# Optimization experiments

Measured on AMD Instinct MI355X. Metric: run time of the kernel, lower is better.

Reference implementation:

```python
import jax, jax.numpy as jnp
import numpy as np
from jax import lax

B, T, C, H = 4, 2048, 512, 8
HD = C // H
FF = 4 * C

def _ln(x, g, b, eps=1e-5):
    m = jnp.mean(x, -1, keepdims=True)
    v = jnp.var(x, -1, keepdims=True)
    return (x - m) * lax.rsqrt(v + eps) * g + b

def setup_inputs():
    key = jax.random.key(0)
    ks = jax.random.split(key, 16)
    n = lambda i, shape, s=0.02: jax.random.normal(ks[i], shape, jnp.float32) * s
    return dict(
        x=jax.random.normal(ks[0], (B, T, C), jnp.float32),
        A=jax.random.uniform(ks[1], (B, T), dtype=jnp.float32),
        alpha_bias=jnp.full((1,), 0.1, jnp.float32),
        dst_alpha=jnp.asarray(0.7, jnp.float32),
        dst_beta=jnp.asarray(0.3, jnp.float32),
        conv1_w=n(2, (C, C, 3)), conv1_b=jnp.zeros((C,), jnp.float32),
        ln1_g=jnp.ones((C,), jnp.float32), ln1_b=jnp.zeros((C,), jnp.float32),
        in_proj_w=n(3, (3 * C, C)), in_proj_b=jnp.zeros((3 * C,), jnp.float32),
        out_w=n(4, (C, C)), out_b=jnp.zeros((C,), jnp.float32),
        ln2_g=jnp.ones((C,), jnp.float32), ln2_b=jnp.zeros((C,), jnp.float32),
        mlp_w1=n(5, (FF, C)), mlp_b1=jnp.zeros((FF,), jnp.float32),
        mlp_w2=n(6, (C, FF)), mlp_b2=jnp.zeros((C,), jnp.float32),
        dsa_ln_g=jnp.ones((C,), jnp.float32), dsa_ln_b=jnp.zeros((C,), jnp.float32),
        dsa_dw=n(7, (C, 1, 3)), dsa_db=jnp.zeros((C,), jnp.float32),
        dsa_pw=n(8, (C, C, 1)), dsa_pb=jnp.zeros((C,), jnp.float32),
    )

def reference(x, A, alpha_bias, dst_alpha, dst_beta, conv1_w, conv1_b, ln1_g, ln1_b,
              in_proj_w, in_proj_b, out_w, out_b, ln2_g, ln2_b,
              mlp_w1, mlp_b1, mlp_w2, mlp_b2,
              dsa_ln_g, dsa_ln_b, dsa_dw, dsa_db, dsa_pw, dsa_pb):
    dn = ('NCH', 'OIH', 'NCH')
    # --- CA branch: conv pre-mix on [B,C,T] with residual ---
    xT = jnp.transpose(x, (0, 2, 1))                       # [B,C,T]
    y = lax.conv_general_dilated(xT, conv1_w, (1,), [(1, 1)], dimension_numbers=dn) + conv1_b[None, :, None]
    Ftc = jnp.transpose(xT + jax.nn.gelu(y, approximate=False), (0, 2, 1))  # [B,T,C]
    h = _ln(Ftc, ln1_g, ln1_b)
    # --- MHA with rank-1 additive boundary bias alpha * A_i A_j (detached) ---
    qkv = h @ in_proj_w.T + in_proj_b
    q, k, v = jnp.split(qkv, 3, axis=-1)
    q = q.reshape(B, T, H, HD)
    k = k.reshape(B, T, H, HD)
    v = v.reshape(B, T, H, HD)
    scores = jnp.einsum('bihd,bjhd->bhij', q, k) / np.float32(np.sqrt(HD))
    M_bias = lax.stop_gradient(A[:, :, None] * A[:, None, :])  # [B,T,T]
    scores = scores + (alpha_bias[0] * M_bias)[:, None]        # broadcast over heads
    p = jax.nn.softmax(scores, axis=-1)
    attn = jnp.einsum('bhij,bjhd->bihd', p, v).reshape(B, T, C)
    attn = attn @ out_w.T + out_b
    Ftc2 = attn + x
    hh = _ln(Ftc2, ln2_g, ln2_b)
    ca_out = jax.nn.gelu(hh @ mlp_w1.T + mlp_b1, approximate=False) @ mlp_w2.T + mlp_b2
    # --- DSA branch: depthwise-separable temporal conv ---
    z = _ln(x, dsa_ln_g, dsa_ln_b)
    zT = jnp.transpose(z, (0, 2, 1))
    z1 = lax.conv_general_dilated(zT, dsa_dw, (1,), [(1, 1)], dimension_numbers=dn, feature_group_count=C) + dsa_db[None, :, None]
    z2 = lax.conv_general_dilated(jax.nn.gelu(z1, approximate=False), dsa_pw, (1,), [(0, 0)], dimension_numbers=dn) + dsa_pb[None, :, None]
    dsa_out = jnp.transpose(z2, (0, 2, 1))
    return dst_alpha * ca_out + dst_beta * dsa_out
```

## Files before the change

kernel.cpp:

```cpp
#include <hip/hip_runtime.h>
#include <cmath>

typedef __attribute__((ext_vector_type(8))) short short8;
typedef __attribute__((ext_vector_type(4))) float floatx4;

#define TT 2048
#define CCH 512
#define MROWS 8192
static const size_t N1 = 4194304;
#define LOG2E 1.44269504088896340736f

__device__ __forceinline__ float gelu_f(float x) {
    return 0.5f * x * (1.0f + erff(x * 0.70710678118654752440f));
}
__device__ __forceinline__ unsigned short f2bf(float x) {
    union { float f; unsigned u; } v; v.f = x;
    unsigned r = v.u + 0x7fffu + ((v.u >> 16) & 1u);
    return (unsigned short)(r >> 16);
}
__device__ __forceinline__ float bf2f(unsigned short h) {
    union { unsigned u; float f; } v; v.u = ((unsigned)h) << 16;
    return v.f;
}
__device__ __forceinline__ unsigned cvtpk(float a, float b) {
    unsigned r;
    asm("v_cvt_pk_bf16_f32 %0, %1, %2" : "=v"(r) : "v"(a), "v"(b));
    return r;
}
__device__ __forceinline__ void gld16(const unsigned short* g, unsigned short* l) {
    __builtin_amdgcn_global_load_lds(
        (const __attribute__((address_space(1))) void*)g,
        (__attribute__((address_space(3))) void*)l, 16, 0, 0);
}

__global__ __launch_bounds__(256)
void pack_w(const float* __restrict__ qkvw, const float* __restrict__ outw,
            const float* __restrict__ w1, const float* __restrict__ w2,
            const float* __restrict__ pw, const float* __restrict__ cv,
            unsigned short* __restrict__ W)
{
    const int idx = blockIdx.x * 256 + threadIdx.x;
    float v;
    if (idx < 786432)            v = qkvw[idx];
    else if (idx < 1048576)      v = outw[idx - 786432];
    else if (idx < 2097152)      v = w1[idx - 1048576];
    else if (idx < 3145728)      v = w2[idx - 2097152];
    else if (idx < 3407872)      v = pw[idx - 3145728];
    else {
        const int l = idx - 3407872;
        const int n = l / 1536, k = l - n * 1536;
        const int ks = k >> 9, ci = k & 511;
        v = cv[n * 1536 + ci * 3 + ks];
    }
    W[idx] = f2bf(v);
}

__global__ __launch_bounds__(256)
void pack_x(const float* __restrict__ x, const float* __restrict__ gam,
            const float* __restrict__ bet, unsigned short* __restrict__ z,
            unsigned short* __restrict__ xpad)
{
    const int m = blockIdx.x, tid = threadIdx.x;
    const int b = m >> 11, t = m & (TT - 1);
    const float2 xv = *(const float2*)&x[(size_t)m * 512 + 2 * tid];
    float s = xv.x + xv.y, sq = xv.x * xv.x + xv.y * xv.y;
    #pragma unroll
    for (int off = 32; off; off >>= 1) { s += __shfl_xor(s, off); sq += __shfl_xor(sq, off); }
    __shared__ float ws[4], wq[4];
    const int wave = tid >> 6, lane = tid & 63;
    if (lane == 0) { ws[wave] = s; wq[wave] = sq; }
    __syncthreads();
    s = ws[0] + ws[1] + ws[2] + ws[3];
    sq = wq[0] + wq[1] + wq[2] + wq[3];
    const float mean = s * (1.0f / 512.0f);
    const float var = sq * (1.0f / 512.0f) - mean * mean;
    const float rstd = rsqrtf(var + 1e-5f);
    const float y0 = (xv.x - mean) * rstd * gam[2 * tid]     + bet[2 * tid];
    const float y1 = (xv.y - mean) * rstd * gam[2 * tid + 1] + bet[2 * tid + 1];
    *(unsigned*)&z[(size_t)m * 512 + 2 * tid] = ((unsigned)f2bf(y1) << 16) | f2bf(y0);
    *(unsigned*)&xpad[((size_t)(b * (TT + 2) + t + 1)) * 512 + 2 * tid] =
        ((unsigned)f2bf(xv.y) << 16) | f2bf(xv.x);
    if (t == 0)
        *(unsigned*)&xpad[((size_t)(b * (TT + 2))) * 512 + 2 * tid] = 0u;
    if (t == TT - 1)
        *(unsigned*)&xpad[((size_t)(b * (TT + 2) + TT + 1)) * 512 + 2 * tid] = 0u;
}

__global__ __launch_bounds__(256)
void ln_bf(const unsigned short* __restrict__ in, const float* __restrict__ gam,
           const float* __restrict__ bet, unsigned short* __restrict__ out)
{
    const int m = blockIdx.x, tid = threadIdx.x;
    const unsigned pv = *(const unsigned*)&in[(size_t)m * 512 + 2 * tid];
    const float x0 = bf2f((unsigned short)pv), x1 = bf2f((unsigned short)(pv >> 16));
    float s = x0 + x1, sq = x0 * x0 + x1 * x1;
    #pragma unroll
    for (int off = 32; off; off >>= 1) { s += __shfl_xor(s, off); sq += __shfl_xor(sq, off); }
    __shared__ float ws[4], wq[4];
    const int wave = tid >> 6, lane = tid & 63;
    if (lane == 0) { ws[wave] = s; wq[wave] = sq; }
    __syncthreads();
    s = ws[0] + ws[1] + ws[2] + ws[3];
    sq = wq[0] + wq[1] + wq[2] + wq[3];
    const float mean = s * (1.0f / 512.0f);
    const float var = sq * (1.0f / 512.0f) - mean * mean;
    const float rstd = rsqrtf(var + 1e-5f);
    const float y0 = (x0 - mean) * rstd * gam[2 * tid]     + bet[2 * tid];
    const float y1 = (x1 - mean) * rstd * gam[2 * tid + 1] + bet[2 * tid + 1];
    *(unsigned*)&out[(size_t)m * 512 + 2 * tid] = ((unsigned)f2bf(y1) << 16) | f2bf(y0);
}

__global__ __launch_bounds__(256)
void dwconv_k(const unsigned short* __restrict__ z, const float* __restrict__ dw,
              const float* __restrict__ db, unsigned short* __restrict__ g)
{
    const int m = blockIdx.x, tid = threadIdx.x, t = m & (TT - 1);
    const int c = 2 * tid;
    const size_t base = (size_t)m * 512 + c;
    const unsigned vm = *(const unsigned*)&z[base];
    const unsigned va = (t > 0)      ? *(const unsigned*)&z[base - 512] : 0u;
    const unsigned vc = (t < TT - 1) ? *(const unsigned*)&z[base + 512] : 0u;
    float y[2];
    #pragma unroll
    for (int j = 0; j < 2; ++j) {
        const float a  = bf2f((unsigned short)(va >> (16 * j)));
        const float bb = bf2f((unsigned short)(vm >> (16 * j)));
        const float cc = bf2f((unsigned short)(vc >> (16 * j)));
        const int ch = c + j;
        y[j] = gelu_f(a * dw[ch * 3] + bb * dw[ch * 3 + 1] + cc * dw[ch * 3 + 2] + db[ch]);
    }
    *(unsigned*)&g[base] = ((unsigned)f2bf(y[1]) << 16) | f2bf(y[0]);
}

template<int EPI, int AF>
__device__ __forceinline__ void gemm_body(
    const unsigned short* __restrict__ A, const unsigned short* __restrict__ Bw,
    const float* __restrict__ bias, const float* __restrict__ resf,
    const unsigned short* __restrict__ dsa,
    const float* __restrict__ sA, const float* __restrict__ sB,
    float* __restrict__ outf, unsigned short* __restrict__ o1,
    unsigned short* __restrict__ o2, unsigned short* __restrict__ o3,
    int Nn, int K, int gx, unsigned short* AsB, unsigned short* BsB)
{
    constexpr int MI = 4, NJ = 2, NBUF = 2;
    constexpr int ASTR = 64 * 32, BSTR = 128 * 32;

    const int nwg = gx * gridDim.y;
    const int orig = blockIdx.x + gx * blockIdx.y;
    const int wg = (orig & 7) * (nwg >> 3) + (orig >> 3);
    const int bx = wg % gx, by = wg / gx;

    const int tid = threadIdx.x;
    const int bm = by * 64, bn = bx * 128;
    const int lane = tid & 63, w = tid >> 6;
    const int wc = w;
    const int lr = lane & 15, g = lane >> 4;

    auto stage = [&](int buf, int k0) {
        unsigned short* Asb = AsB + buf * ASTR;
        unsigned short* Bsb = BsB + buf * BSTR;
        {
            const int c = tid;
            const int r = c >> 2, c8 = c & 3;
            const int c8s = c8 ^ ((r >> 1) & 3);
            const unsigned short* src;
            if (AF == 1) {
                const int m = bm + r;
                const int b = m >> 11, t = m & (TT - 1);
                const int k = k0 + c8s * 8;
                const int ks = k >> 9, ci = k & 511;
                src = A + ((size_t)(b * (TT + 2) + t + ks) * 512 + ci);
            } else {
                src = A + ((size_t)(bm + r) * K + k0 + c8s * 8);
            }
            gld16(src, Asb + (size_t)c * 8);
        }
        #pragma unroll
        for (int i = 0; i < 2; ++i) {
            const int c = tid + i * 256;
            const int r = c >> 2, c8 = c & 3;
            const int c8s = c8 ^ ((r >> 1) & 3);
            gld16(Bw + ((size_t)(bn + r) * K + k0 + c8s * 8), Bsb + (size_t)c * 8);
        }
    };

    floatx4 acc[MI][NJ];
    #pragma unroll
    for (int mi = 0; mi < MI; ++mi)
        #pragma unroll
        for (int nj = 0; nj < NJ; ++nj)
            acc[mi][nj] = (floatx4){0.f, 0.f, 0.f, 0.f};

    const int nt = K >> 5;
    stage(0, 0);
    __syncthreads();
    int cur = 0;
    for (int t = 0; t < nt; ++t) {
        if (t + 1 < nt) stage(cur ^ 1, (t + 1) * 32);

        const unsigned short* Asb = AsB + cur * ASTR;
        const unsigned short* Bsb = BsB + cur * BSTR;
        short8 av[MI], bv[NJ];
        #pragma unroll
        for (int mi = 0; mi < MI; ++mi) {
            const int row = mi * 16 + lr;
            av[mi] = *(const short8*)&Asb[row * 32 + (g ^ ((row >> 1) & 3)) * 8];
        }
        #pragma unroll
        for (int nj = 0; nj < NJ; ++nj) {
            const int row = wc * 32 + nj * 16 + lr;
            bv[nj] = *(const short8*)&Bsb[row * 32 + (g ^ ((row >> 1) & 3)) * 8];
        }
        __builtin_amdgcn_s_setprio(1);
        #pragma unroll
        for (int mi = 0; mi < MI; ++mi)
            #pragma unroll
            for (int nj = 0; nj < NJ; ++nj)
                acc[mi][nj] = __builtin_amdgcn_mfma_f32_16x16x32_bf16(av[mi], bv[nj], acc[mi][nj], 0, 0, 0);
        __builtin_amdgcn_s_setprio(0);
        __syncthreads();
        cur ^= 1;
    }

    float sa = 0.f, sb = 0.f;
    if (EPI == 5) { sa = sA[0]; sb = sB[0]; }
    #pragma unroll
    for (int mi = 0; mi < MI; ++mi)
        #pragma unroll
        for (int nj = 0; nj < NJ; ++nj)
            #pragma unroll
            for (int reg = 0; reg < 4; ++reg) {
                const int m = bm + mi * 16 + g * 4 + reg;
                const int n = bn + wc * 32 + nj * 16 + lr;
                float v = acc[mi][nj][reg] + bias[n];
                if (EPI == 0) {
                    const int b = m >> 11, t = m & (TT - 1);
                    if (n < 512) {
                        o1[(size_t)m * 512 + n] = f2bf(v * (0.125f * LOG2E));
                    } else if (n < 1024) {
                        o2[(size_t)m * 512 + (n - 512)] = f2bf(v);
                    } else {
                        const int c = n - 1024;
                        o3[(size_t)(b * 8 + (c >> 6)) * 64 * TT + (size_t)(c & 63) * TT + t] = f2bf(v);
                    }
                } else if (EPI == 1) {
                    o1[(size_t)m * 512 + n] = f2bf(v);
                } else if (EPI == 2) {
                    o1[(size_t)m * 512 + n] = f2bf(resf[(size_t)m * 512 + n] + gelu_f(v));
                } else if (EPI == 3) {
                    o1[(size_t)m * 512 + n] = f2bf(v + resf[(size_t)m * 512 + n]);
                } else if (EPI == 4) {
                    o1[(size_t)m * Nn + n] = f2bf(gelu_f(v));
                } else {
                    outf[(size_t)m * 512 + n] = sa * v + sb * bf2f(dsa[(size_t)m * 512 + n]);
                }
            }
}

template<int EPI, int AF>
__global__ __launch_bounds__(256, 4)
void gemm_k(const unsigned short* __restrict__ A, const unsigned short* __restrict__ Bw,
            const float* __restrict__ bias, const float* __restrict__ resf,
            const unsigned short* __restrict__ dsa,
            const float* __restrict__ sA, const float* __restrict__ sB,
            float* __restrict__ outf, unsigned short* __restrict__ o1,
            unsigned short* __restrict__ o2, unsigned short* __restrict__ o3,
            int Nn, int K)
{
    __shared__ unsigned short As[2 * 64 * 32];
    __shared__ unsigned short Bs[2 * 128 * 32];
    gemm_body<EPI, AF>(A, Bw, bias, resf, dsa, sA, sB, outf, o1, o2, o3,
                       Nn, K, gridDim.x, As, Bs);
}

__global__ __launch_bounds__(256, 4)
void gemm_dual(const unsigned short* __restrict__ Gb, const unsigned short* __restrict__ Wpw,
               const float* __restrict__ dsa_pb, unsigned short* __restrict__ Db,
               const unsigned short* __restrict__ xpad, const unsigned short* __restrict__ Wcv,
               const float* __restrict__ conv1_b, const float* __restrict__ x,
               unsigned short* __restrict__ U1)
{
    __shared__ unsigned short As[2 * 64 * 32];
    __shared__ unsigned short Bs[2 * 128 * 32];
    if (blockIdx.z == 0)
        gemm_body<1, 0>(Gb, Wpw, dsa_pb, nullptr, nullptr, nullptr, nullptr,
                        nullptr, Db, nullptr, nullptr, 512, 512, gridDim.x, As, Bs);
    else
        gemm_body<2, 1>(xpad, Wcv, conv1_b, x, nullptr, nullptr, nullptr,
                        nullptr, U1, nullptr, nullptr, 512, 1536, gridDim.x, As, Bs);
}

__global__ __launch_bounds__(512, 2)
void attn_k(const unsigned short* __restrict__ Qb, const unsigned short* __restrict__ Kb,
            const unsigned short* __restrict__ Vtg, const float* __restrict__ Avec,
            const float* __restrict__ alpha_p, unsigned short* __restrict__ Oh)
{
    __shared__ unsigned short Kt[2][2][64 * 64];
    __shared__ unsigned short Vt[2][2][64 * 64];
    __shared__ unsigned short P2[8][16 * 64];

    const int tid = threadIdx.x;
    const int w = tid >> 6, lane = tid & 63;
    const int lr = lane & 15, g = lane >> 4;
    const int i0 = blockIdx.x * 128;
    const int h = blockIdx.y, b = blockIdx.z;
    const float* Ab = Avec + b * TT;
    const int q_glob = i0 + w * 16 + lr;
    const float aqs = alpha_p[0] * LOG2E * Ab[q_glob];

    const int j_s = tid >> 3, c8_s = tid & 7;

    short8 kreg[2], vreg[2];
    auto load_tiles = [&](int kv0) {
        #pragma unroll
        for (int i = 0; i < 2; ++i) {
            kreg[i] = *(const short8*)&Kb[(size_t)(b * TT + kv0 + i * 64 + j_s) * 512 + h * 64 + c8_s * 8];
            vreg[i] = *(const short8*)&Vtg[(size_t)((b * 8 + h) * 64 + j_s) * TT + kv0 + i * 64 + c8_s * 8];
        }
    };
    auto write_tiles = [&](int buf) {
        const int off = j_s * 64 + (((c8_s * 16) ^ ((j_s & 7) << 4)) >> 1);
        #pragma unroll
        for (int i = 0; i < 2; ++i) {
            *(short8*)&Kt[buf][i][off] = kreg[i];
            *(short8*)&Vt[buf][i][off] = vreg[i];
        }
    };

    short8 qf[2];
    #pragma unroll
    for (int kk = 0; kk < 2; ++kk)
        qf[kk] = *(const short8*)&Qb[(size_t)(b * TT + q_glob) * 512 + h * 64 + kk * 32 + g * 8];

    float l_part = 0.f;
    floatx4 o[4];
    #pragma unroll
    for (int fd = 0; fd < 4; ++fd) o[fd] = (floatx4){0.f, 0.f, 0.f, 0.f};

    load_tiles(0);
    write_tiles(0);
    __syncthreads();
    int cur = 0;

    for (int t = 0; t < 16; ++t) {
        if (t < 15) load_tiles((t + 1) * 128);

        #pragma unroll
        for (int st = 0; st < 2; ++st) {
            const int kv0 = t * 128 + st * 64;

            floatx4 akv[4];
            #pragma unroll
            for (int fc = 0; fc < 4; ++fc)
                akv[fc] = *(const floatx4*)&Ab[kv0 + fc * 16 + g * 4];

            floatx4 s[4];
            #pragma unroll
            for (int fc = 0; fc < 4; ++fc) {
                const int row = fc * 16 + lr;
                const short8 kf0 = *(const short8*)&Kt[cur][st][row * 64 + (((g * 16) ^ ((row & 7) << 4)) >> 1)];
                const short8 kf1 = *(const short8*)&Kt[cur][st][row * 64 + (((64 + g * 16) ^ ((row & 7) << 4)) >> 1)];
                floatx4 tacc = (floatx4){0.f, 0.f, 0.f, 0.f};
                __builtin_amdgcn_s_setprio(1);
                tacc = __builtin_amdgcn_mfma_f32_16x16x32_bf16(kf0, qf[0], tacc, 0, 0, 0);
                tacc = __builtin_amdgcn_mfma_f32_16x16x32_bf16(kf1, qf[1], tacc, 0, 0, 0);
                __builtin_amdgcn_s_setprio(0);
                s[fc] = tacc;
            }
            #pragma unroll
            for (int fc = 0; fc < 4; ++fc)
                #pragma unroll
                for (int r = 0; r < 4; ++r) {
                    const float p = exp2f(s[fc][r] + aqs * akv[fc][r]);
                    s[fc][r] = p;
                    l_part += p;
                }

            #pragma unroll
            for (int fc = 0; fc < 4; ++fc) {
                uint2 pk;
                pk.x = cvtpk(s[fc][0], s[fc][1]);
                pk.y = cvtpk(s[fc][2], s[fc][3]);
                const int boff = (lr * 128 + fc * 32 + g * 8) ^ ((lr & 7) << 4);
                *(uint2*)((char*)&P2[w][0] + boff) = pk;
            }
            short8 pf[2];
            #pragma unroll
            for (int kk = 0; kk < 2; ++kk) {
                const int boff = (lr * 128 + kk * 64 + g * 16) ^ ((lr & 7) << 4);
                pf[kk] = *(const short8*)((const char*)&P2[w][0] + boff);
            }
            #pragma unroll
            for (int fd = 0; fd < 4; ++fd) {
                const int row = fd * 16 + lr;
                const short8 vf0 = *(const short8*)&Vt[cur][st][row * 64 + (((g * 16) ^ ((row & 7) << 4)) >> 1)];
                const short8 vf1 = *(const short8*)&Vt[cur][st][row * 64 + (((64 + g * 16) ^ ((row & 7) << 4)) >> 1)];
                __builtin_amdgcn_s_setprio(1);
                o[fd] = __builtin_amdgcn_mfma_f32_16x16x32_bf16(vf0, pf[0], o[fd], 0, 0, 0);
                o[fd] = __builtin_amdgcn_mfma_f32_16x16x32_bf16(vf1, pf[1], o[fd], 0, 0, 0);
                __builtin_amdgcn_s_setprio(0);
            }
        }

        if (t < 15) write_tiles(cur ^ 1);
        __syncthreads();
        cur ^= 1;
    }

    l_part += __shfl_xor(l_part, 16);
    l_part += __shfl_xor(l_part, 32);
    const float inv = 1.0f / l_part;
    const size_t orow = (size_t)(b * TT + q_glob) * 512 + h * 64;
    #pragma unroll
    for (int fd = 0; fd < 4; ++fd) {
        uint2 pk;
        pk.x = cvtpk(o[fd][0] * inv, o[fd][1] * inv);
        pk.y = cvtpk(o[fd][2] * inv, o[fd][3] * inv);
        *(uint2*)&Oh[orow + fd * 16 + g * 4] = pk;
    }
}

extern "C" void kernel_launch(void* const* d_in, const int* in_sizes, int n_in,
                              void* d_out, int out_size, void* d_ws, size_t ws_size,
                              hipStream_t stream)
{
    const float* x         = (const float*)d_in[0];
    const float* Avec      = (const float*)d_in[1];
    const float* alpha_b   = (const float*)d_in[2];
    const float* dst_alpha = (const float*)d_in[3];
    const float* dst_beta  = (const float*)d_in[4];
    const float* conv1_w   = (const float*)d_in[5];
    const float* conv1_b   = (const float*)d_in[6];
    const float* ln1_g     = (const float*)d_in[7];
    const float* ln1_b     = (const float*)d_in[8];
    const float* in_proj_w = (const float*)d_in[9];
    const float* in_proj_b = (const float*)d_in[10];
    const float* out_w     = (const float*)d_in[11];
    const float* out_b     = (const float*)d_in[12];
    const float* ln2_g     = (const float*)d_in[13];
    const float* ln2_b     = (const float*)d_in[14];
    const float* mlp_w1    = (const float*)d_in[15];
    const float* mlp_b1    = (const float*)d_in[16];
    const float* mlp_w2    = (const float*)d_in[17];
    const float* mlp_b2    = (const float*)d_in[18];
    const float* dsa_ln_g  = (const float*)d_in[19];
    const float* dsa_ln_b  = (const float*)d_in[20];
    const float* dsa_dw    = (const float*)d_in[21];
    const float* dsa_db    = (const float*)d_in[22];
    const float* dsa_pw    = (const float*)d_in[23];
    const float* dsa_pb    = (const float*)d_in[24];

    unsigned short* W    = (unsigned short*)d_ws;
    unsigned short* xpad = W + N1;
    unsigned short* Qb   = xpad + (size_t)4 * (TT + 2) * 512;
    unsigned short* Kbf  = Qb + N1;
    unsigned short* Vt   = Kbf + N1;
    unsigned short* Zb   = Vt + N1;
    unsigned short* Tb   = Qb;
    unsigned short* Gb   = Zb + N1;
    unsigned short* Db   = Gb + N1;
    unsigned short* U1   = Db + N1;
    unsigned short* U2   = U1 + N1;
    unsigned short* U3   = U2 + N1;

    const int off_qkv = 0, off_out = 786432, off_w1 = 1048576,
              off_w2 = 2097152, off_pw = 3145728, off_cv = 3407872;

    pack_w<<<16384, 256, 0, stream>>>(in_proj_w, out_w, mlp_w1, mlp_w2, dsa_pw, conv1_w, W);
    pack_x<<<MROWS, 256, 0, stream>>>(x, dsa_ln_g, dsa_ln_b, Zb, xpad);

    dwconv_k<<<MROWS, 256, 0, stream>>>(Zb, dsa_dw, dsa_db, Gb);
    gemm_dual<<<dim3(4, 128, 2), 256, 0, stream>>>(Gb, W + off_pw, dsa_pb, Db,
        xpad, W + off_cv, conv1_b, x, U1);
    ln_bf<<<MROWS, 256, 0, stream>>>(U1, ln1_g, ln1_b, U2);

    gemm_k<0, 0><<<dim3(12, 128), 256, 0, stream>>>(U2, W + off_qkv, in_proj_b,
        nullptr, nullptr, nullptr, nullptr, nullptr, Qb, Kbf, Vt, 1536, 512);

    attn_k<<<dim3(16, 8, 4), 512, 0, stream>>>(Qb, Kbf, Vt, Avec, alpha_b, U1);

    gemm_k<3, 0><<<dim3(4, 128), 256, 0, stream>>>(U1, W + off_out, out_b,
        x, nullptr, nullptr, nullptr, nullptr, U3, nullptr, nullptr, 512, 512);
    ln_bf<<<MROWS, 256, 0, stream>>>(U3, ln2_g, ln2_b, U2);

    gemm_k<4, 0><<<dim3(16, 128), 256, 0, stream>>>(U2, W + off_w1, mlp_b1,
        nullptr, nullptr, nullptr, nullptr, nullptr, Tb, nullptr, nullptr, 2048, 512);
    gemm_k<5, 0><<<dim3(4, 128), 256, 0, stream>>>(Tb, W + off_w2, mlp_b2,
        nullptr, Db, dst_alpha, dst_beta, (float*)d_out, nullptr, nullptr, nullptr,
        512, 2048);
}
```

Baseline: 258.7 us.

## Add 128-row GEMM tile for QKV and MLP1, precompute attention LDS offsets

Templates the GEMM on an M-tile size so the QKV and first MLP projections use 128x128 tiles with a 2x2 warp layout (each warp computing 64x64), which raises operand reuse per LDS load and halves the number of workgroups. The attention kernel now computes its swizzled LDS fragment offsets and global K/V/A pointers once and advances pointers each tile instead of recomputing addresses in the inner loop. The larger tile raises accumulator register use and LDS footprint under the same launch bounds, which may cut occupancy or cause spills, and with fewer workgroups the tail effects change.

```diff
diff --git a/kernel.cpp b/kernel.cpp
--- a/kernel.cpp
+++ b/kernel.cpp
@@ -132,7 +132,7 @@
     *(unsigned*)&g[base] = ((unsigned)f2bf(y[1]) << 16) | f2bf(y[0]);
 }
 
-template<int EPI, int AF>
+template<int EPI, int AF, int TM>
 __device__ __forceinline__ void gemm_body(
     const unsigned short* __restrict__ A, const unsigned short* __restrict__ Bw,
     const float* __restrict__ bias, const float* __restrict__ resf,
@@ -142,8 +142,10 @@
     unsigned short* __restrict__ o2, unsigned short* __restrict__ o3,
     int Nn, int K, int gx, unsigned short* AsB, unsigned short* BsB)
 {
-    constexpr int MI = 4, NJ = 2, NBUF = 2;
-    constexpr int ASTR = 64 * 32, BSTR = 128 * 32;
+    constexpr int WC = (TM == 128) ? 2 : 4;
+    constexpr int MI = 4;
+    constexpr int NJ = (TM == 128) ? 4 : 2;
+    constexpr int ASTR = TM * 32, BSTR = 128 * 32;
 
     const int nwg = gx * gridDim.y;
     const int orig = blockIdx.x + gx * blockIdx.y;
@@ -151,16 +153,17 @@
     const int bx = wg % gx, by = wg / gx;
 
     const int tid = threadIdx.x;
-    const int bm = by * 64, bn = bx * 128;
+    const int bm = by * TM, bn = bx * 128;
     const int lane = tid & 63, w = tid >> 6;
-    const int wc = w;
+    const int wr = w / WC, wc = w % WC;
     const int lr = lane & 15, g = lane >> 4;
 
     auto stage = [&](int buf, int k0) {
         unsigned short* Asb = AsB + buf * ASTR;
         unsigned short* Bsb = BsB + buf * BSTR;
-        {
-            const int c = tid;
+        #pragma unroll
+        for (int i = 0; i < TM / 64; ++i) {
+            const int c = tid + i * 256;
             const int r = c >> 2, c8 = c & 3;
             const int c8s = c8 ^ ((r >> 1) & 3);
             const unsigned short* src;
@@ -203,12 +206,12 @@
         short8 av[MI], bv[NJ];
         #pragma unroll
         for (int mi = 0; mi < MI; ++mi) {
-            const int row = mi * 16 + lr;
+            const int row = wr * (MI * 16) + mi * 16 + lr;
             av[mi] = *(const short8*)&Asb[row * 32 + (g ^ ((row >> 1) & 3)) * 8];
         }
         #pragma unroll
         for (int nj = 0; nj < NJ; ++nj) {
-            const int row = wc * 32 + nj * 16 + lr;
+            const int row = wc * (NJ * 16) + nj * 16 + lr;
             bv[nj] = *(const short8*)&Bsb[row * 32 + (g ^ ((row >> 1) & 3)) * 8];
         }
         __builtin_amdgcn_s_setprio(1);
@@ -230,8 +233,8 @@
         for (int nj = 0; nj < NJ; ++nj)
             #pragma unroll
             for (int reg = 0; reg < 4; ++reg) {
-                const int m = bm + mi * 16 + g * 4 + reg;
-                const int n = bn + wc * 32 + nj * 16 + lr;
+                const int m = bm + wr * (MI * 16) + mi * 16 + g * 4 + reg;
+                const int n = bn + wc * (NJ * 16) + nj * 16 + lr;
                 float v = acc[mi][nj][reg] + bias[n];
                 if (EPI == 0) {
                     const int b = m >> 11, t = m & (TT - 1);
@@ -257,7 +260,7 @@
             }
 }
 
-template<int EPI, int AF>
+template<int EPI, int AF, int TM>
 __global__ __launch_bounds__(256, 4)
 void gemm_k(const unsigned short* __restrict__ A, const unsigned short* __restrict__ Bw,
             const float* __restrict__ bias, const float* __restrict__ resf,
@@ -267,10 +270,10 @@
             unsigned short* __restrict__ o2, unsigned short* __restrict__ o3,
             int Nn, int K)
 {
-    __shared__ unsigned short As[2 * 64 * 32];
+    __shared__ unsigned short As[2 * TM * 32];
     __shared__ unsigned short Bs[2 * 128 * 32];
-    gemm_body<EPI, AF>(A, Bw, bias, resf, dsa, sA, sB, outf, o1, o2, o3,
-                       Nn, K, gridDim.x, As, Bs);
+    gemm_body<EPI, AF, TM>(A, Bw, bias, resf, dsa, sA, sB, outf, o1, o2, o3,
+                           Nn, K, gridDim.x, As, Bs);
 }
 
 __global__ __launch_bounds__(256, 4)
@@ -283,11 +286,11 @@
     __shared__ unsigned short As[2 * 64 * 32];
     __shared__ unsigned short Bs[2 * 128 * 32];
     if (blockIdx.z == 0)
-        gemm_body<1, 0>(Gb, Wpw, dsa_pb, nullptr, nullptr, nullptr, nullptr,
-                        nullptr, Db, nullptr, nullptr, 512, 512, gridDim.x, As, Bs);
+        gemm_body<1, 0, 64>(Gb, Wpw, dsa_pb, nullptr, nullptr, nullptr, nullptr,
+                            nullptr, Db, nullptr, nullptr, 512, 512, gridDim.x, As, Bs);
     else
-        gemm_body<2, 1>(xpad, Wcv, conv1_b, x, nullptr, nullptr, nullptr,
-                        nullptr, U1, nullptr, nullptr, 512, 1536, gridDim.x, As, Bs);
+        gemm_body<2, 1, 64>(xpad, Wcv, conv1_b, x, nullptr, nullptr, nullptr,
+                            nullptr, U1, nullptr, nullptr, 512, 1536, gridDim.x, As, Bs);
 }
 
 __global__ __launch_bounds__(512, 2)
@@ -308,22 +311,44 @@
     const int q_glob = i0 + w * 16 + lr;
     const float aqs = alpha_p[0] * LOG2E * Ab[q_glob];
 
+    int fOff[4][2];
+    #pragma unroll
+    for (int f = 0; f < 4; ++f) {
+        const int row = f * 16 + lr;
+        #pragma unroll
+        for (int kk = 0; kk < 2; ++kk)
+            fOff[f][kk] = row * 64 + (((kk * 64 + g * 16) ^ ((row & 7) << 4)) >> 1);
+    }
+    int pwOff[4], prOff[2];
+    #pragma unroll
+    for (int fc = 0; fc < 4; ++fc)
+        pwOff[fc] = (lr * 128 + fc * 32 + g * 8) ^ ((lr & 7) << 4);
+    #pragma unroll
+    for (int kk = 0; kk < 2; ++kk)
+        prOff[kk] = (lr * 128 + kk * 64 + g * 16) ^ ((lr & 7) << 4);
+
     const int j_s = tid >> 3, c8_s = tid & 7;
+    const int wOff = j_s * 64 + (((c8_s * 16) ^ ((j_s & 7) << 4)) >> 1);
+
+    const unsigned short* kP = Kb + (size_t)(b * TT + j_s) * 512 + h * 64 + c8_s * 8;
+    const unsigned short* vP = Vtg + (size_t)((b * 8 + h) * 64 + j_s) * TT + c8_s * 8;
+    const float* aP = Ab + g * 4;
 
     short8 kreg[2], vreg[2];
-    auto load_tiles = [&](int kv0) {
+    auto load_tiles = [&]() {
         #pragma unroll
         for (int i = 0; i < 2; ++i) {
-            kreg[i] = *(const short8*)&Kb[(size_t)(b * TT + kv0 + i * 64 + j_s) * 512 + h * 64 + c8_s * 8];
-            vreg[i] = *(const short8*)&Vtg[(size_t)((b * 8 + h) * 64 + j_s) * TT + kv0 + i * 64 + c8_s * 8];
-        }
+            kreg[i] = *(const short8*)(kP + (size_t)i * 64 * 512);
+            vreg[i] = *(const short8*)(vP + i * 64);
+        }
+        kP += (size_t)128 * 512;
+        vP += 128;
     };
     auto write_tiles = [&](int buf) {
-        const int off = j_s * 64 + (((c8_s * 16) ^ ((j_s & 7) << 4)) >> 1);
         #pragma unroll
         for (int i = 0; i < 2; ++i) {
-            *(short8*)&Kt[buf][i][off] = kreg[i];
-            *(short8*)&Vt[buf][i][off] = vreg[i];
+            *(short8*)&Kt[buf][i][wOff] = kreg[i];
+            *(short8*)&Vt[buf][i][wOff] = vreg[i];
         }
     };
 
@@ -337,29 +362,30 @@
     #pragma unroll
     for (int fd = 0; fd < 4; ++fd) o[fd] = (floatx4){0.f, 0.f, 0.f, 0.f};
 
-    load_tiles(0);
+    load_tiles();
     write_tiles(0);
     __syncthreads();
     int cur = 0;
 
     for (int t = 0; t < 16; ++t) {
-        if (t < 15) load_tiles((t + 1) * 128);
+        if (t < 15) load_tiles();
 
         #pragma unroll
         for (int st = 0; st < 2; ++st) {
-            const int kv0 = t * 128 + st * 64;
+            const unsigned short* ktb = &Kt[cur][st][0];
+            const unsigned short* vtb = &Vt[cur][st][0];
 
             floatx4 akv[4];
             #pragma unroll
             for (int fc = 0; fc < 4; ++fc)
-                akv[fc] = *(const floatx4*)&Ab[kv0 + fc * 16 + g * 4];
+                akv[fc] = *(const floatx4*)(aP + fc * 16);
+            aP += 64;
 
             floatx4 s[4];
             #pragma unroll
             for (int fc = 0; fc < 4; ++fc) {
-                const int row = fc * 16 + lr;
-                const short8 kf0 = *(const short8*)&Kt[cur][st][row * 64 + (((g * 16) ^ ((row & 7) << 4)) >> 1)];
-                const short8 kf1 = *(const short8*)&Kt[cur][st][row * 64 + (((64 + g * 16) ^ ((row & 7) << 4)) >> 1)];
+                const short8 kf0 = *(const short8*)&ktb[fOff[fc][0]];
+                const short8 kf1 = *(const short8*)&ktb[fOff[fc][1]];
                 floatx4 tacc = (floatx4){0.f, 0.f, 0.f, 0.f};
                 __builtin_amdgcn_s_setprio(1);
                 tacc = __builtin_amdgcn_mfma_f32_16x16x32_bf16(kf0, qf[0], tacc, 0, 0, 0);
@@ -381,20 +407,16 @@
                 uint2 pk;
                 pk.x = cvtpk(s[fc][0], s[fc][1]);
                 pk.y = cvtpk(s[fc][2], s[fc][3]);
-                const int boff = (lr * 128 + fc * 32 + g * 8) ^ ((lr & 7) << 4);
-                *(uint2*)((char*)&P2[w][0] + boff) = pk;
+                *(uint2*)((char*)&P2[w][0] + pwOff[fc]) = pk;
             }
             short8 pf[2];
             #pragma unroll
-            for (int kk = 0; kk < 2; ++kk) {
-                const int boff = (lr * 128 + kk * 64 + g * 16) ^ ((lr & 7) << 4);
-                pf[kk] = *(const short8*)((const char*)&P2[w][0] + boff);
-            }
+            for (int kk = 0; kk < 2; ++kk)
+                pf[kk] = *(const short8*)((const char*)&P2[w][0] + prOff[kk]);
             #pragma unroll
             for (int fd = 0; fd < 4; ++fd) {
-                const int row = fd * 16 + lr;
-                const short8 vf0 = *(const short8*)&Vt[cur][st][row * 64 + (((g * 16) ^ ((row & 7) << 4)) >> 1)];
-                const short8 vf1 = *(const short8*)&Vt[cur][st][row * 64 + (((64 + g * 16) ^ ((row & 7) << 4)) >> 1)];
+                const short8 vf0 = *(const short8*)&vtb[fOff[fd][0]];
+                const short8 vf1 = *(const short8*)&vtb[fOff[fd][1]];
                 __builtin_amdgcn_s_setprio(1);
                 o[fd] = __builtin_amdgcn_mfma_f32_16x16x32_bf16(vf0, pf[0], o[fd], 0, 0, 0);
                 o[fd] = __builtin_amdgcn_mfma_f32_16x16x32_bf16(vf1, pf[1], o[fd], 0, 0, 0);
@@ -474,18 +496,18 @@
         xpad, W + off_cv, conv1_b, x, U1);
     ln_bf<<<MROWS, 256, 0, stream>>>(U1, ln1_g, ln1_b, U2);
 
-    gemm_k<0, 0><<<dim3(12, 128), 256, 0, stream>>>(U2, W + off_qkv, in_proj_b,
+    gemm_k<0, 0, 128><<<dim3(12, 64), 256, 0, stream>>>(U2, W + off_qkv, in_proj_b,
         nullptr, nullptr, nullptr, nullptr, nullptr, Qb, Kbf, Vt, 1536, 512);
 
     attn_k<<<dim3(16, 8, 4), 512, 0, stream>>>(Qb, Kbf, Vt, Avec, alpha_b, U1);
 
-    gemm_k<3, 0><<<dim3(4, 128), 256, 0, stream>>>(U1, W + off_out, out_b,
+    gemm_k<3, 0, 64><<<dim3(4, 128), 256, 0, stream>>>(U1, W + off_out, out_b,
         x, nullptr, nullptr, nullptr, nullptr, U3, nullptr, nullptr, 512, 512);
     ln_bf<<<MROWS, 256, 0, stream>>>(U3, ln2_g, ln2_b, U2);
 
-    gemm_k<4, 0><<<dim3(16, 128), 256, 0, stream>>>(U2, W + off_w1, mlp_b1,
+    gemm_k<4, 0, 128><<<dim3(16, 64), 256, 0, stream>>>(U2, W + off_w1, mlp_b1,
         nullptr, nullptr, nullptr, nullptr, nullptr, Tb, nullptr, nullptr, 2048, 512);
-    gemm_k<5, 0><<<dim3(4, 128), 256, 0, stream>>>(Tb, W + off_w2, mlp_b2,
+    gemm_k<5, 0, 64><<<dim3(4, 128), 256, 0, stream>>>(Tb, W + off_w2, mlp_b2,
         nullptr, Db, dst_alpha, dst_beta, (float*)d_out, nullptr, nullptr, nullptr,
         512, 2048);
 }
```

Result: slower. 281.9 us (+9.0%).
